# Performance work log

Measured on AMD Instinct MI355X. Metric: run time of the kernel, lower is better.

Reference implementation:

```python
import jax, jax.numpy as jnp
import numpy as np

D, L, W, K = 16, 1000000, 64, 8
PAD = (W - 1) // 2  # 31, matches padding1 in the torch code


def setup_inputs() -> dict:
    key = jax.random.key(0)
    kx, kp = jax.random.split(key)
    x = jax.random.normal(kx, (D, L), dtype=jnp.float32)
    # torch uses torch.rand (uniform [0,1)) for each of the K (D,W) parameters
    P = jax.random.uniform(kp, (K, D, W), dtype=jnp.float32)
    return {"x": x, "P": P}


def _fullscan(x, P):
    # x: (D, L); P: (K, D, W)
    p = PAD
    # --- middle positions k in [p, L-W+p]: standard valid correlation ---
    # mid[k_out, o] = sum_{d,m} x[d, o+m] * P[k_out, d, m], position k = o + p
    mid = jax.lax.conv_general_dilated(
        x[None],                      # (1, D, L)
        P,                            # (K, D, W)
        window_strides=(1,),
        padding="VALID",
        dimension_numbers=("NCH", "OIH", "NCH"),
    )[0]                              # (K, L-W+1)
    # --- left edge k in [0, p): data x[:, :k+W-p] * kernel[:, :k+W-p] ---
    # prefix[i, m] = sum_d x[d, m] * P[i, d, m] over the first W samples
    tl = jnp.einsum("dm,kdm->km", x[:, :W], P)        # (K, W)
    left_c = jnp.cumsum(tl, axis=1)                    # prefix sums
    left = left_c[:, W - p - 1 : W - 1]                # (K, p)
    # --- right edge k in (L-W+p, L): data x[:, k-p:] * kernel[:, W+k-L-p:] ---
    tr = jnp.einsum("dm,kdm->km", x[:, L - W :], P)    # (K, W)
    suf = jnp.cumsum(tr[:, ::-1], axis=1)[:, ::-1]     # suffix sums: suf[:, t] = sum_{m>=t}
    right = suf[:, 1 : W - p]                          # (K, W-1-p)
    y = jnp.concatenate([left, mid, right], axis=1)    # (K, L)
    return y.reshape(-1, 1)                            # (K*L, 1)


def reference(x, P):
    return _fullscan(x, P)
```

## Files before the change

### kernel.cpp

```cpp
#include <hip/hip_runtime.h>


constexpr int D    = 16;
constexpr int L    = 1000000;
constexpr int W    = 64;
constexpr int K    = 8;
constexpr int PADL = 31;
constexpr int NMID = L - W + 1;
constexpr int TPB  = 256;
constexpr int OTW  = 8;
constexpr int CTW  = OTW + 2;
constexpr int BLK_OUT = 4 * OTW * 32;
constexpr int XS   = 1104;
constexpr int NQ   = XS / 4;
constexpr int NBLK = (NMID + BLK_OUT - 1) / BLK_OUT;
constexpr int NGRID = NBLK + K;

typedef __attribute__((ext_vector_type(8)))  short short8;
typedef __attribute__((ext_vector_type(16))) float floatx16;

__device__ __forceinline__ unsigned short f2bf(float f) {
    union { float f; unsigned u; } v; v.f = f;
    unsigned u = v.u + 0x7fff + ((v.u >> 16) & 1);
    return (unsigned short)(u >> 16);
}

__device__ __forceinline__ unsigned long long pack4(float a, float b,
                                                    float c, float d) {
    return (unsigned long long)f2bf(a)
         | ((unsigned long long)f2bf(b) << 16)
         | ((unsigned long long)f2bf(c) << 32)
         | ((unsigned long long)f2bf(d) << 48);
}

__global__ __launch_bounds__(TPB, 3) void fullscan_mid(
    const float* __restrict__ x, const float* __restrict__ P,
    const unsigned short* __restrict__ afr, float* __restrict__ out)
{
    __shared__ __align__(16) unsigned short xs[XS * 16];
    const int bid = blockIdx.x;
    const int tid = threadIdx.x;

    if (bid >= NBLK) {
        const int k = bid - NBLK;
        const int j = tid;
        if (j < PADL) {
            float acc = 0.0f;
            for (int m = 0; m <= 32 + j; ++m)
#pragma unroll
                for (int d = 0; d < D; ++d)
                    acc = fmaf(x[d * L + m], P[(k * D + d) * W + m], acc);
            out[k * L + j] = acc;
        } else if (j < 2 * PADL + 1) {
            const int jj = j - PADL;
            float acc = 0.0f;
            for (int m = jj + 1; m < W; ++m)
#pragma unroll
                for (int d = 0; d < D; ++d)
                    acc = fmaf(x[d * L + (L - W) + m], P[(k * D + d) * W + m], acc);
            out[k * L + PADL + NMID + jj] = acc;
        }
        return;
    }

    const int s0   = bid * BLK_OUT;
    const int lane = tid & 63;
    const int wv   = tid >> 6;

    {
        const int pl = tid & 63;
        const int dq = tid >> 6;
        if (s0 + XS <= L) {
            const float4* xq0 = (const float4*)(x + (4 * dq + 0) * L + s0);
            const float4* xq1 = (const float4*)(x + (4 * dq + 1) * L + s0);
            const float4* xq2 = (const float4*)(x + (4 * dq + 2) * L + s0);
            const float4* xq3 = (const float4*)(x + (4 * dq + 3) * L + s0);
#pragma unroll 2
            for (int it = 0; it < 5; ++it) {
                const int q = it * 64 + pl;
                if (q < NQ) {
                    const float4 v0 = xq0[q];
                    const float4 v1 = xq1[q];
                    const float4 v2 = xq2[q];
                    const float4 v3 = xq3[q];
                    const int rot = q & 3;
                    unsigned short* base = &xs[q * 64 + dq * 4];
                    *(unsigned long long*)(base + (0 ^ rot) * 16) = pack4(v0.x, v1.x, v2.x, v3.x);
                    *(unsigned long long*)(base + (1 ^ rot) * 16) = pack4(v0.y, v1.y, v2.y, v3.y);
                    *(unsigned long long*)(base + (2 ^ rot) * 16) = pack4(v0.z, v1.z, v2.z, v3.z);
                    *(unsigned long long*)(base + (3 ^ rot) * 16) = pack4(v0.w, v1.w, v2.w, v3.w);
                }
            }
        } else {
            const float* xr0 = x + (4 * dq + 0) * L + s0;
            const float* xr1 = x + (4 * dq + 1) * L + s0;
            const float* xr2 = x + (4 * dq + 2) * L + s0;
            const float* xr3 = x + (4 * dq + 3) * L + s0;
#pragma unroll 1
            for (int b = 0; b < XS; b += 64) {
                const int pos = b + pl;
                if (pos < XS) {
                    const bool ok = (s0 + pos) < L;
                    const float v0 = ok ? xr0[pos] : 0.0f;
                    const float v1 = ok ? xr1[pos] : 0.0f;
                    const float v2 = ok ? xr2[pos] : 0.0f;
                    const float v3 = ok ? xr3[pos] : 0.0f;
                    const int idx = (pos * 16 + dq * 4) ^ (((pos >> 2) & 3) << 4);
                    *(unsigned long long*)&xs[idx] = pack4(v0, v1, v2, v3);
                }
            }
        }
    }

    short8 A[16];
#pragma unroll
    for (int c = 0; c < 16; ++c)
        A[c] = *(const short8*)(afr + (c * 64 + lane) * 8);

    __syncthreads();

    const int n  = lane & 31;
    const int h  = lane >> 5;
    const int hb = h * 8;
    const int wbase = wv * OTW;

    float pendA[4], pendB[4], prev4[4], prev12[4];

#pragma unroll
    for (int jj = 0; jj < CTW; ++jj) {
        floatx16 acc;
#pragma unroll
        for (int r = 0; r < 16; ++r) acc[r] = 0.0f;
        const int p0 = (wbase + jj) * 32 + n;

        short8 Bc[4], Bn[4];
#pragma unroll
        for (int u = 0; u < 4; ++u) {
            const int pos = p0 + u;
            Bc[u] = *(const short8*)&xs[(pos * 16 + hb) ^ (((pos >> 2) & 3) << 4)];
        }
#pragma unroll
        for (int u = 0; u < 4; ++u) {
            const int pos = p0 + 4 + u;
            Bn[u] = *(const short8*)&xs[(pos * 16 + hb) ^ (((pos >> 2) & 3) << 4)];
        }
#pragma unroll
        for (int u = 0; u < 4; ++u)
            acc = __builtin_amdgcn_mfma_f32_32x32x16_bf16(A[u], Bc[u], acc, 0, 0, 0);
#pragma unroll
        for (int u = 0; u < 4; ++u) {
            const int pos = p0 + 8 + u;
            Bc[u] = *(const short8*)&xs[(pos * 16 + hb) ^ (((pos >> 2) & 3) << 4)];
        }
#pragma unroll
        for (int u = 0; u < 4; ++u)
            acc = __builtin_amdgcn_mfma_f32_32x32x16_bf16(A[4 + u], Bn[u], acc, 0, 0, 0);
#pragma unroll
        for (int u = 0; u < 4; ++u) {
            const int pos = p0 + 12 + u;
            Bn[u] = *(const short8*)&xs[(pos * 16 + hb) ^ (((pos >> 2) & 3) << 4)];
        }
#pragma unroll
        for (int u = 0; u < 4; ++u)
            acc = __builtin_amdgcn_mfma_f32_32x32x16_bf16(A[8 + u], Bc[u], acc, 0, 0, 0);
#pragma unroll
        for (int u = 0; u < 4; ++u)
            acc = __builtin_amdgcn_mfma_f32_32x32x16_bf16(A[12 + u], Bn[u], acc, 0, 0, 0);

        if (jj >= 2) {
            const int ot = jj - 2;
            const int t = s0 + (wbase + ot) * 32 + n;
#pragma unroll
            for (int kk = 0; kk < 4; ++kk) {
                const float g3t = (n >= 16) ? prev12[kk] : acc[kk + 12];
                const float v = pendA[kk] + __shfl_xor(g3t, 16, 64);
                if (t < NMID)
                    out[(kk + 4 * h) * L + PADL + t] = v;
            }
        }
        if (jj >= 1) {
#pragma unroll
            for (int kk = 0; kk < 4; ++kk) {
                const float g1t = (n >= 16) ? prev4[kk] : acc[kk + 4];
                pendA[kk] = pendB[kk] + acc[kk + 8] + __shfl_xor(g1t, 16, 64);
            }
        }
#pragma unroll
        for (int kk = 0; kk < 4; ++kk) {
            pendB[kk]  = acc[kk];
            prev4[kk]  = acc[kk + 4];
            prev12[kk] = acc[kk + 12];
        }
    }
}

__global__ void fullscan_prep(const float* __restrict__ P,
                              unsigned short* __restrict__ afr)
{
    const int u = blockIdx.x * 256 + threadIdx.x;
    const int c = u >> 9, lane = (u >> 3) & 63, j = u & 7;
    const int m = lane & 31, h = lane >> 5;
    const int k = m & 7, g = m >> 3;
    const int d = 8 * h + j;
    const int w = 16 * g + c;
    afr[u] = f2bf(P[(k * D + d) * W + w]);
}

extern "C" void kernel_launch(void* const* d_in, const int* in_sizes, int n_in,
                              void* d_out, int out_size, void* d_ws, size_t ws_size,
                              hipStream_t stream)
{
    const float* x = (const float*)d_in[0];
    const float* P = (const float*)d_in[1];
    float* out = (float*)d_out;
    unsigned short* afr = (unsigned short*)d_ws;

    hipLaunchKernelGGL(fullscan_prep, dim3(32), dim3(256), 0, stream, P, afr);
    hipLaunchKernelGGL(fullscan_mid, dim3(NGRID), dim3(TPB), 0, stream,
                       x, P, afr, out);
}
```

Before: 134.1 us.

## Give each wave its own x tile slice to drop the block barrier

Each wavefront now stages into shared memory only the 84 position-quads that its own MFMA tiles read, for all 16 channels. Previously the whole block loaded the tile cooperatively. Because no wave reads LDS data written by another wave, the __syncthreads before the compute loop is removed, so waves can start compute as soon as their own loads land. The cost is redundant global loads and bf16 conversion for the overlapping halo between adjacent waves, plus narrower 256-byte contiguous segments per row.

After: 134.4 us. Within noise of the previous version (+0.2%).

```diff
diff --git a/kernel.cpp b/kernel.cpp
--- a/kernel.cpp
+++ b/kernel.cpp
@@ -13,6 +13,7 @@
 constexpr int BLK_OUT = 4 * OTW * 32;
 constexpr int XS   = 1104;
 constexpr int NQ   = XS / 4;
+constexpr int QPW  = 84;
 constexpr int NBLK = (NMID + BLK_OUT - 1) / BLK_OUT;
 constexpr int NGRID = NBLK + K;
 
@@ -68,23 +69,24 @@
     const int wv   = tid >> 6;
 
     {
-        const int pl = tid & 63;
-        const int dq = tid >> 6;
+        const int pq  = lane & 15;
+        const int dqw = lane >> 4;
         if (s0 + XS <= L) {
-            const float4* xq0 = (const float4*)(x + (4 * dq + 0) * L + s0);
-            const float4* xq1 = (const float4*)(x + (4 * dq + 1) * L + s0);
-            const float4* xq2 = (const float4*)(x + (4 * dq + 2) * L + s0);
-            const float4* xq3 = (const float4*)(x + (4 * dq + 3) * L + s0);
+            const float4* xq0 = (const float4*)(x + (4 * dqw + 0) * L + s0);
+            const float4* xq1 = (const float4*)(x + (4 * dqw + 1) * L + s0);
+            const float4* xq2 = (const float4*)(x + (4 * dqw + 2) * L + s0);
+            const float4* xq3 = (const float4*)(x + (4 * dqw + 3) * L + s0);
 #pragma unroll 2
-            for (int it = 0; it < 5; ++it) {
-                const int q = it * 64 + pl;
-                if (q < NQ) {
+            for (int it = 0; it < 6; ++it) {
+                const int qrel = it * 16 + pq;
+                if (qrel < QPW) {
+                    const int q = wv * 64 + qrel;
                     const float4 v0 = xq0[q];
                     const float4 v1 = xq1[q];
                     const float4 v2 = xq2[q];
                     const float4 v3 = xq3[q];
                     const int rot = q & 3;
-                    unsigned short* base = &xs[q * 64 + dq * 4];
+                    unsigned short* base = &xs[q * 64 + dqw * 4];
                     *(unsigned long long*)(base + (0 ^ rot) * 16) = pack4(v0.x, v1.x, v2.x, v3.x);
                     *(unsigned long long*)(base + (1 ^ rot) * 16) = pack4(v0.y, v1.y, v2.y, v3.y);
                     *(unsigned long long*)(base + (2 ^ rot) * 16) = pack4(v0.z, v1.z, v2.z, v3.z);
@@ -92,21 +94,28 @@
                 }
             }
         } else {
-            const float* xr0 = x + (4 * dq + 0) * L + s0;
-            const float* xr1 = x + (4 * dq + 1) * L + s0;
-            const float* xr2 = x + (4 * dq + 2) * L + s0;
-            const float* xr3 = x + (4 * dq + 3) * L + s0;
+            const float* xr0 = x + (4 * dqw + 0) * L + s0;
+            const float* xr1 = x + (4 * dqw + 1) * L + s0;
+            const float* xr2 = x + (4 * dqw + 2) * L + s0;
+            const float* xr3 = x + (4 * dqw + 3) * L + s0;
 #pragma unroll 1
-            for (int b = 0; b < XS; b += 64) {
-                const int pos = b + pl;
-                if (pos < XS) {
-                    const bool ok = (s0 + pos) < L;
-                    const float v0 = ok ? xr0[pos] : 0.0f;
-                    const float v1 = ok ? xr1[pos] : 0.0f;
-                    const float v2 = ok ? xr2[pos] : 0.0f;
-                    const float v3 = ok ? xr3[pos] : 0.0f;
-                    const int idx = (pos * 16 + dq * 4) ^ (((pos >> 2) & 3) << 4);
-                    *(unsigned long long*)&xs[idx] = pack4(v0, v1, v2, v3);
+            for (int it = 0; it < 6; ++it) {
+                const int qrel = it * 16 + pq;
+                if (qrel < QPW) {
+                    const int q = wv * 64 + qrel;
+                    const int rot = q & 3;
+                    unsigned short* base = &xs[q * 64 + dqw * 4];
+#pragma unroll
+                    for (int j = 0; j < 4; ++j) {
+                        const int pos = 4 * q + j;
+                        const bool ok = (s0 + pos) < L;
+                        const float v0 = ok ? xr0[pos] : 0.0f;
+                        const float v1 = ok ? xr1[pos] : 0.0f;
+                        const float v2 = ok ? xr2[pos] : 0.0f;
+                        const float v3 = ok ? xr3[pos] : 0.0f;
+                        *(unsigned long long*)(base + (j ^ rot) * 16) =
+                            pack4(v0, v1, v2, v3);
+                    }
                 }
             }
         }
@@ -117,7 +126,6 @@
     for (int c = 0; c < 16; ++c)
         A[c] = *(const short8*)(afr + (c * 64 + lane) * 8);
 
-    __syncthreads();
 
     const int n  = lane & 31;
     const int h  = lane >> 5;
```

## Fold weight prep into main kernel and rework LDS swizzle for staging

Applied to the files above, without the earlier changes.

Removes the separate prep kernel launch by having every block gather and convert its MFMA A-fragments directly from P in global memory. It also changes the shared-memory swizzle to a one-bit XOR within each 16-element row and remaps the staging thread order so that LDS stores avoid bank conflicts. The cost is redundant strided global gathers of P in every block (128 scalar loads per lane), which mostly hit cache, in exchange for one fewer launch and cheaper staging writes.

Measured after the change: 138.1 us. 1.03x slower.

```diff
diff --git a/kernel.cpp b/kernel.cpp
--- a/kernel.cpp
+++ b/kernel.cpp
@@ -13,6 +13,7 @@
 constexpr int BLK_OUT = 4 * OTW * 32;
 constexpr int XS   = 1104;
 constexpr int NQ   = XS / 4;
+constexpr int SIT  = (NQ + 63) / 64;
 constexpr int NBLK = (NMID + BLK_OUT - 1) / BLK_OUT;
 constexpr int NGRID = NBLK + K;
 
@@ -33,9 +34,13 @@
          | ((unsigned long long)f2bf(d) << 48);
 }
 
+__device__ __forceinline__ float selx(const float4 v, int j) {
+    return j == 0 ? v.x : j == 1 ? v.y : j == 2 ? v.z : v.w;
+}
+
 __global__ __launch_bounds__(TPB, 3) void fullscan_mid(
     const float* __restrict__ x, const float* __restrict__ P,
-    const unsigned short* __restrict__ afr, float* __restrict__ out)
+    float* __restrict__ out)
 {
     __shared__ __align__(16) unsigned short xs[XS * 16];
     const int bid = blockIdx.x;
@@ -70,25 +75,30 @@
     {
         const int pl = tid & 63;
         const int dq = tid >> 6;
+        const int qrel = (pl >> 2) + (pl & 3) * 16;
         if (s0 + XS <= L) {
             const float4* xq0 = (const float4*)(x + (4 * dq + 0) * L + s0);
             const float4* xq1 = (const float4*)(x + (4 * dq + 1) * L + s0);
             const float4* xq2 = (const float4*)(x + (4 * dq + 2) * L + s0);
             const float4* xq3 = (const float4*)(x + (4 * dq + 3) * L + s0);
 #pragma unroll 2
-            for (int it = 0; it < 5; ++it) {
-                const int q = it * 64 + pl;
+            for (int it = 0; it < SIT; ++it) {
+                const int q = it * 64 + qrel;
                 if (q < NQ) {
                     const float4 v0 = xq0[q];
                     const float4 v1 = xq1[q];
                     const float4 v2 = xq2[q];
                     const float4 v3 = xq3[q];
-                    const int rot = q & 3;
-                    unsigned short* base = &xs[q * 64 + dq * 4];
-                    *(unsigned long long*)(base + (0 ^ rot) * 16) = pack4(v0.x, v1.x, v2.x, v3.x);
-                    *(unsigned long long*)(base + (1 ^ rot) * 16) = pack4(v0.y, v1.y, v2.y, v3.y);
-                    *(unsigned long long*)(base + (2 ^ rot) * 16) = pack4(v0.z, v1.z, v2.z, v3.z);
-                    *(unsigned long long*)(base + (3 ^ rot) * 16) = pack4(v0.w, v1.w, v2.w, v3.w);
+                    const int swz = q & 1;
+#pragma unroll
+                    for (int i = 0; i < 4; ++i) {
+                        const int j = (i + pl) & 3;
+                        const int pos = 4 * q + j;
+                        *(unsigned long long*)
+                            &xs[pos * 16 + ((dq * 4) ^ (swz * 8))] =
+                            pack4(selx(v0, j), selx(v1, j),
+                                  selx(v2, j), selx(v3, j));
+                    }
                 }
             }
         } else {
@@ -105,17 +115,25 @@
                     const float v1 = ok ? xr1[pos] : 0.0f;
                     const float v2 = ok ? xr2[pos] : 0.0f;
                     const float v3 = ok ? xr3[pos] : 0.0f;
-                    const int idx = (pos * 16 + dq * 4) ^ (((pos >> 2) & 3) << 4);
-                    *(unsigned long long*)&xs[idx] = pack4(v0, v1, v2, v3);
+                    const int swz = (pos >> 2) & 1;
+                    *(unsigned long long*)&xs[pos * 16 + ((dq * 4) ^ (swz * 8))] =
+                        pack4(v0, v1, v2, v3);
                 }
             }
         }
     }
 
     short8 A[16];
-#pragma unroll
-    for (int c = 0; c < 16; ++c)
-        A[c] = *(const short8*)(afr + (c * 64 + lane) * 8);
+    {
+        const int m = lane & 31, hA = lane >> 5;
+        const int k = m & 7, g = m >> 3;
+        const float* Pb = P + ((k * D + 8 * hA) * W + 16 * g);
+#pragma unroll
+        for (int c = 0; c < 16; ++c)
+#pragma unroll
+            for (int j = 0; j < 8; ++j)
+                A[c][j] = (short)f2bf(Pb[j * W + c]);
+    }
 
     __syncthreads();
 
@@ -133,39 +151,29 @@
         for (int r = 0; r < 16; ++r) acc[r] = 0.0f;
         const int p0 = (wbase + jj) * 32 + n;
 
+#define BRD(pos) (*(const short8*)&xs[(pos) * 16 + (hb ^ ((((pos) >> 2) & 1) * 8))])
         short8 Bc[4], Bn[4];
 #pragma unroll
-        for (int u = 0; u < 4; ++u) {
-            const int pos = p0 + u;
-            Bc[u] = *(const short8*)&xs[(pos * 16 + hb) ^ (((pos >> 2) & 3) << 4)];
-        }
-#pragma unroll
-        for (int u = 0; u < 4; ++u) {
-            const int pos = p0 + 4 + u;
-            Bn[u] = *(const short8*)&xs[(pos * 16 + hb) ^ (((pos >> 2) & 3) << 4)];
-        }
+        for (int u = 0; u < 4; ++u) Bc[u] = BRD(p0 + u);
+#pragma unroll
+        for (int u = 0; u < 4; ++u) Bn[u] = BRD(p0 + 4 + u);
 #pragma unroll
         for (int u = 0; u < 4; ++u)
             acc = __builtin_amdgcn_mfma_f32_32x32x16_bf16(A[u], Bc[u], acc, 0, 0, 0);
 #pragma unroll
-        for (int u = 0; u < 4; ++u) {
-            const int pos = p0 + 8 + u;
-            Bc[u] = *(const short8*)&xs[(pos * 16 + hb) ^ (((pos >> 2) & 3) << 4)];
-        }
+        for (int u = 0; u < 4; ++u) Bc[u] = BRD(p0 + 8 + u);
 #pragma unroll
         for (int u = 0; u < 4; ++u)
             acc = __builtin_amdgcn_mfma_f32_32x32x16_bf16(A[4 + u], Bn[u], acc, 0, 0, 0);
 #pragma unroll
-        for (int u = 0; u < 4; ++u) {
-            const int pos = p0 + 12 + u;
-            Bn[u] = *(const short8*)&xs[(pos * 16 + hb) ^ (((pos >> 2) & 3) << 4)];
-        }
+        for (int u = 0; u < 4; ++u) Bn[u] = BRD(p0 + 12 + u);
 #pragma unroll
         for (int u = 0; u < 4; ++u)
             acc = __builtin_amdgcn_mfma_f32_32x32x16_bf16(A[8 + u], Bc[u], acc, 0, 0, 0);
 #pragma unroll
         for (int u = 0; u < 4; ++u)
             acc = __builtin_amdgcn_mfma_f32_32x32x16_bf16(A[12 + u], Bn[u], acc, 0, 0, 0);
+#undef BRD
 
         if (jj >= 2) {
             const int ot = jj - 2;
@@ -192,18 +200,6 @@
             prev12[kk] = acc[kk + 12];
         }
     }
-}
-
-__global__ void fullscan_prep(const float* __restrict__ P,
-                              unsigned short* __restrict__ afr)
-{
-    const int u = blockIdx.x * 256 + threadIdx.x;
-    const int c = u >> 9, lane = (u >> 3) & 63, j = u & 7;
-    const int m = lane & 31, h = lane >> 5;
-    const int k = m & 7, g = m >> 3;
-    const int d = 8 * h + j;
-    const int w = 16 * g + c;
-    afr[u] = f2bf(P[(k * D + d) * W + w]);
 }
 
 extern "C" void kernel_launch(void* const* d_in, const int* in_sizes, int n_in,
@@ -213,9 +209,7 @@
     const float* x = (const float*)d_in[0];
     const float* P = (const float*)d_in[1];
     float* out = (float*)d_out;
-    unsigned short* afr = (unsigned short*)d_ws;
-
-    hipLaunchKernelGGL(fullscan_prep, dim3(32), dim3(256), 0, stream, P, afr);
+
     hipLaunchKernelGGL(fullscan_mid, dim3(NGRID), dim3(TPB), 0, stream,
-                       x, P, afr, out);
-}
+                       x, P, out);
+}
```
